# Performance work log

Hardware: AMD Instinct MI355X
Metric: run time of the kernel (lower is better)

## Reference

```python
import jax, jax.numpy as jnp
import numpy as np

FILTERS = 512
DQK = FILTERS // 8  # 64


def setup_inputs() -> dict:
    key = jax.random.key(0)
    ks = jax.random.split(key, 7)
    B, H, W, C = 32, 32, 32, FILTERS
    x = jax.random.normal(ks[0], (B, H, W, C), dtype=jnp.float32)
    # 1x1 convs == per-pixel dense layers: weight [Cin, Cout], bias [Cout]
    def glorot(k, cin, cout):
        lim = np.sqrt(6.0 / (cin + cout)).astype(np.float32)
        return jax.random.uniform(k, (cin, cout), jnp.float32, -lim, lim)
    return {
        "x": x,
        "wq": glorot(ks[1], C, DQK), "bq": jnp.zeros((DQK,), jnp.float32),
        "wk": glorot(ks[2], C, DQK), "bk": jnp.zeros((DQK,), jnp.float32),
        "wv": glorot(ks[3], C, C),   "bv": jnp.zeros((C,), jnp.float32),
    }


def reference(x, wq, bq, wk, bk, wv, bv):
    B, H, W, C = x.shape
    N = H * W
    xf = x.reshape(B, N, C)                       # flatten spatial -> tokens
    q = xf @ wq + bq                              # [B, N, C//8]
    k = xf @ wk + bk                              # [B, N, C//8]
    v = xf @ wv + bv                              # [B, N, C]
    scale = 1.0 / jnp.sqrt(jnp.float32(C // 8))
    scores = jnp.einsum('bnd,bmd->bnm', q, k) * scale  # [B, N, N]
    probs = jax.nn.softmax(scores, axis=-1)
    attended = jnp.einsum('bnm,bmc->bnc', probs, v)    # [B, N, C]
    return attended.reshape(B, H, W, C) + x
```

## Files before the change

### kernel.cpp

```cpp
#include <hip/hip_runtime.h>
#include <stdint.h>

#define B_ 32
#define N_ 1024
#define C_ 512
#define D_ 64

typedef __attribute__((ext_vector_type(8))) __bf16 bf8;
typedef __attribute__((ext_vector_type(4))) float f32x4;

typedef const __attribute__((address_space(1))) void* gp_t;
typedef __attribute__((address_space(3))) void* lp_t;

__device__ inline void g2l16(const void* g, void* l) {
    __builtin_amdgcn_global_load_lds((gp_t)g, (lp_t)l, 16, 0, 0);
}

__device__ inline float b2f(unsigned short u) {
    return __uint_as_float(((unsigned)u) << 16);
}
__device__ inline unsigned short f2b(float f) {
    unsigned u = __float_as_uint(f);
    u += 0x7FFF + ((u >> 16) & 1);
    return (unsigned short)(u >> 16);
}

#define MFMA16(a, b, c) __builtin_amdgcn_mfma_f32_16x16x32_bf16((a), (b), (c), 0, 0, 0)

__device__ __forceinline__ void ld_frags(const unsigned short* As, const unsigned short* Bs,
                                         int wm, int wn, int lane,
                                         bf8 (&a)[2][4], bf8 (&bb)[2][4]) {
    #pragma unroll
    for (int kq = 0; kq < 2; ++kq) {
        #pragma unroll
        for (int ti = 0; ti < 4; ++ti)
            a[kq][ti] = *(const bf8*)&As[((wm * 4 + ti) * 2 + kq) * 512 + lane * 8];
        #pragma unroll
        for (int tj = 0; tj < 4; ++tj)
            bb[kq][tj] = *(const bf8*)&Bs[((wn * 4 + tj) * 2 + kq) * 512 + lane * 8];
    }
}

__device__ __forceinline__ void do_mfma(const bf8 (&a)[2][4], const bf8 (&bb)[2][4],
                                        f32x4 (&acc)[4][4]) {
    #pragma unroll
    for (int kq = 0; kq < 2; ++kq)
        #pragma unroll
        for (int ti = 0; ti < 4; ++ti)
            #pragma unroll
            for (int tj = 0; tj < 4; ++tj)
                acc[ti][tj] = MFMA16(a[kq][ti], bb[kq][tj], acc[ti][tj]);
}

__global__ __launch_bounds__(256) void xcvt(const float* __restrict__ x,
                                            unsigned short* __restrict__ xb) {
    int i = blockIdx.x * 256 + threadIdx.x;
    float4 f = ((const float4*)x)[i];
    ushort4 o;
    o.x = f2b(f.x); o.y = f2b(f.y); o.z = f2b(f.z); o.w = f2b(f.w);
    ((ushort4*)xb)[i] = o;
}

__global__ __launch_bounds__(256) void wtrans_all(
    const float* __restrict__ wq, const float* __restrict__ wk,
    const float* __restrict__ wv, unsigned short* __restrict__ wt)
{
    int t = blockIdx.x * 256 + threadIdx.x;
    int co = t >> 9;
    int ci = t & 511;
    const float* src;
    int col, cout;
    if (co < 64)       { src = wq; col = co;       cout = 64;  }
    else if (co < 128) { src = wk; col = co - 64;  cout = 64;  }
    else               { src = wv; col = co - 128; cout = 512; }
    wt[t] = f2b(src[(size_t)ci * cout + col]);
}

__global__ __launch_bounds__(256) void qkv(
    const unsigned short* __restrict__ xb,
    const unsigned short* __restrict__ WT,
    const float* __restrict__ bq, const float* __restrict__ bk,
    const float* __restrict__ bv,
    unsigned short* __restrict__ q, unsigned short* __restrict__ k,
    unsigned short* __restrict__ vT)
{
    const int f_  = blockIdx.x;
    const int xcd = f_ & 7;
    const int s_  = f_ >> 3;
    const int rb  = xcd * 32 + s_ / 5;
    const int cb  = s_ % 5;

    const int tid = threadIdx.x;
    const int lane = tid & 63;
    const int wave = tid >> 6;
    const int wm = wave >> 1, wn = wave & 1;
    const int lr = lane & 15;
    const int lk = lane >> 4;

    __shared__ unsigned short SM[32768];
    unsigned short* TB = SM;

    const int row0 = rb * 128;
    const int col0 = cb * 128;

    f32x4 zero4 = {0.f, 0.f, 0.f, 0.f};
    f32x4 acc[4][4];
    #pragma unroll
    for (int i = 0; i < 4; ++i)
        #pragma unroll
        for (int j = 0; j < 4; ++j) acc[i][j] = zero4;

    auto stage = [&](int buf, int kk) {
        unsigned short* As = SM + buf * 8192;
        unsigned short* Bs = SM + 16384 + buf * 8192;
        #pragma unroll
        for (int i = 0; i < 4; ++i) {
            int f = wave * 4 + i;
            int t = f >> 1, kq = f & 1;
            g2l16(xb + (size_t)(row0 + t * 16 + lr) * C_ + kk + kq * 32 + lk * 8,
                  &As[f * 512]);
            g2l16(WT + (size_t)(col0 + t * 16 + lr) * C_ + kk + kq * 32 + lk * 8,
                  &Bs[f * 512]);
        }
    };

    stage(0, 0);
    stage(1, 64);
    int cur = 0;
    for (int t = 0; t < 6; ++t) {
        asm volatile("s_waitcnt vmcnt(8)" ::: "memory");
        __builtin_amdgcn_s_barrier();
        bf8 a[2][4], bb[2][4];
        ld_frags(SM + cur * 8192, SM + 16384 + cur * 8192, wm, wn, lane, a, bb);
        asm volatile("s_waitcnt lgkmcnt(0)" ::: "memory");
        __builtin_amdgcn_s_barrier();
        stage(cur, (t + 2) * 64);
        do_mfma(a, bb, acc);
        cur ^= 1;
    }
    {
        asm volatile("s_waitcnt vmcnt(8)" ::: "memory");
        __builtin_amdgcn_s_barrier();
        bf8 a[2][4], bb[2][4];
        ld_frags(SM + cur * 8192, SM + 16384 + cur * 8192, wm, wn, lane, a, bb);
        do_mfma(a, bb, acc);
        cur ^= 1;
    }
    {
        asm volatile("s_waitcnt vmcnt(0)" ::: "memory");
        __builtin_amdgcn_s_barrier();
        bf8 a[2][4], bb[2][4];
        ld_frags(SM + cur * 8192, SM + 16384 + cur * 8192, wm, wn, lane, a, bb);
        do_mfma(a, bb, acc);
    }

    if (cb == 0) {
        unsigned short* outp = (wn == 0) ? q : k;
        const float* bias = (wn == 0) ? bq : bk;
        #pragma unroll
        for (int ti = 0; ti < 4; ++ti)
            #pragma unroll
            for (int tj = 0; tj < 4; ++tj) {
                int col = tj * 16 + lr;
                float bi = bias[col];
                #pragma unroll
                for (int r = 0; r < 4; ++r) {
                    int row = row0 + wm * 64 + ti * 16 + lk * 4 + r;
                    outp[(size_t)row * D_ + col] = f2b(acc[ti][tj][r] + bi);
                }
            }
    } else {
        const int colv = (cb - 1) * 128;
        __syncthreads();
        #pragma unroll
        for (int ti = 0; ti < 4; ++ti)
            #pragma unroll
            for (int tj = 0; tj < 4; ++tj) {
                int c = wn * 64 + tj * 16 + lr;
                float bi = bv[colv + c];
                int tok = wm * 64 + ti * 16 + lk * 4;
                ushort4 o;
                o.x = f2b(acc[ti][tj][0] + bi);
                o.y = f2b(acc[ti][tj][1] + bi);
                o.z = f2b(acc[ti][tj][2] + bi);
                o.w = f2b(acc[ti][tj][3] + bi);
                *(ushort4*)&TB[c * 132 + tok] = o;
            }
        __syncthreads();
        const int b  = row0 >> 10;
        const int n0 = row0 & 1023;
        #pragma unroll
        for (int i = 0; i < 16; ++i) {
            int idx = tid + 256 * i;
            int c = idx >> 5, ch = idx & 31;
            ushort4 t4 = *(const ushort4*)&TB[c * 132 + ch * 4];
            *(ushort4*)&vT[((size_t)(b * C_ + colv + c)) * N_ + n0 + ch * 4] = t4;
        }
    }
}

#define SLD 1032
__global__ __launch_bounds__(256) void scores(
    const unsigned short* __restrict__ q,
    const unsigned short* __restrict__ k,
    unsigned short* __restrict__ P)
{
    const int f_  = blockIdx.x;
    const int xcd = f_ & 7;
    const int s_  = f_ >> 3;
    const int b   = xcd * 4 + (s_ >> 6);
    const int qt  = s_ & 63;

    const int tid = threadIdx.x, lane = tid & 63, wave = tid >> 6;
    const int lr = lane & 15, lk = lane >> 4;
    __shared__ unsigned short S[16 * SLD];

    const int n0 = qt * 16;
    const unsigned short* qrow = q + (size_t)(b * N_ + n0 + lr) * D_ + lk * 8;
    bf8 qa0 = *(const bf8*)(qrow);
    bf8 qa1 = *(const bf8*)(qrow + 32);

    const int m0w = wave * 256;
    #pragma unroll 4
    for (int mt = 0; mt < 16; ++mt) {
        int m = m0w + mt * 16;
        const unsigned short* krow = k + (size_t)(b * N_ + m + lr) * D_ + lk * 8;
        bf8 kb0 = *(const bf8*)(krow);
        bf8 kb1 = *(const bf8*)(krow + 32);
        f32x4 s = {0.f, 0.f, 0.f, 0.f};
        s = MFMA16(qa0, kb0, s);
        s = MFMA16(qa1, kb1, s);
        #pragma unroll
        for (int r = 0; r < 4; ++r)
            S[(lk * 4 + r) * SLD + m + lr] = f2b(s[r] * 0.125f);
    }
    __syncthreads();

    #pragma unroll
    for (int rr4 = 0; rr4 < 4; ++rr4) {
        int rr = wave * 4 + rr4;
        float vals[16];
        float mx = -1e30f;
        #pragma unroll
        for (int j = 0; j < 16; ++j) {
            vals[j] = b2f(S[rr * SLD + j * 64 + lane]);
            mx = fmaxf(mx, vals[j]);
        }
        #pragma unroll
        for (int off = 32; off; off >>= 1) mx = fmaxf(mx, __shfl_xor(mx, off));
        float sum = 0.f;
        #pragma unroll
        for (int j = 0; j < 16; ++j) { vals[j] = __expf(vals[j] - mx); sum += vals[j]; }
        #pragma unroll
        for (int off = 32; off; off >>= 1) sum += __shfl_xor(sum, off);
        float inv = 1.f / sum;
        unsigned short* pp = P + (size_t)(b * N_ + n0 + rr) * N_;
        #pragma unroll
        for (int j = 0; j < 16; ++j) pp[j * 64 + lane] = f2b(vals[j] * inv);
    }
}

__global__ __launch_bounds__(512, 2) void pv(
    const unsigned short* __restrict__ P,
    const unsigned short* __restrict__ vT,
    const float* __restrict__ x,
    float* __restrict__ out)
{
    const int f_   = blockIdx.x;
    const int xcd  = f_ & 7;
    const int s_   = f_ >> 3;
    const int b    = xcd * 4 + (s_ >> 3);
    const int w_   = s_ & 7;
    const int m0   = (w_ & 3) * 256;
    const int c0   = (w_ >> 2) * 256;

    const int tid = threadIdx.x, lane = tid & 63, wave = tid >> 6;
    const int wm = wave >> 2;
    const int wn = wave & 3;
    const int lr = lane & 15, lk = lane >> 4;

    __shared__ unsigned short SM[65536];

    f32x4 zero4 = {0.f, 0.f, 0.f, 0.f};
    f32x4 acc[8][4];
    #pragma unroll
    for (int i = 0; i < 8; ++i)
        #pragma unroll
        for (int j = 0; j < 4; ++j) acc[i][j] = zero4;

    const unsigned short* Pb = P  + (size_t)b * N_ * N_;
    const unsigned short* Vb = vT + (size_t)b * C_ * N_;

    auto stage = [&](int t32) {
        unsigned short* As = SM + (t32 & 3) * 16384;
        unsigned short* Bs = As + 8192;
        const int kk = t32 * 32;
        #pragma unroll
        for (int i = 0; i < 2; ++i) {
            int f = wave * 2 + i;
            g2l16(Pb + (size_t)(m0 + f * 16 + lr) * N_ + kk + lk * 8, &As[f * 512]);
            g2l16(Vb + (size_t)(c0 + f * 16 + lr) * N_ + kk + lk * 8, &Bs[f * 512]);
        }
    };

    auto compute = [&](int t32) {
        const unsigned short* As = SM + (t32 & 3) * 16384;
        const unsigned short* Bs = As + 8192;
        bf8 a[8], bb[4];
        #pragma unroll
        for (int ti = 0; ti < 8; ++ti)
            a[ti] = *(const bf8*)&As[(wm * 8 + ti) * 512 + lane * 8];
        #pragma unroll
        for (int tj = 0; tj < 4; ++tj)
            bb[tj] = *(const bf8*)&Bs[(wn * 4 + tj) * 512 + lane * 8];
        asm volatile("s_waitcnt lgkmcnt(0)" ::: "memory");
        __builtin_amdgcn_sched_barrier(0);
        __builtin_amdgcn_s_setprio(1);
        #pragma unroll
        for (int ti = 0; ti < 8; ++ti)
            #pragma unroll
            for (int tj = 0; tj < 4; ++tj)
                acc[ti][tj] = MFMA16(a[ti], bb[tj], acc[ti][tj]);
        __builtin_amdgcn_s_setprio(0);
    };

    stage(0); stage(1); stage(2);
    for (int t = 0; t < 29; ++t) {
        asm volatile("s_waitcnt vmcnt(8)" ::: "memory");
        __builtin_amdgcn_s_barrier();
        stage(t + 3);
        compute(t);
    }
    {
        asm volatile("s_waitcnt vmcnt(8)" ::: "memory");
        __builtin_amdgcn_s_barrier();
        compute(29);
    }
    {
        asm volatile("s_waitcnt vmcnt(4)" ::: "memory");
        __builtin_amdgcn_s_barrier();
        compute(30);
    }
    {
        asm volatile("s_waitcnt vmcnt(0)" ::: "memory");
        __builtin_amdgcn_s_barrier();
        compute(31);
    }

    #pragma unroll
    for (int ti = 0; ti < 8; ++ti)
        #pragma unroll
        for (int tj = 0; tj < 4; ++tj) {
            int col = c0 + wn * 64 + tj * 16 + lr;
            #pragma unroll
            for (int r = 0; r < 4; ++r) {
                int row = m0 + wm * 128 + ti * 16 + lk * 4 + r;
                size_t idx = (size_t)(b * N_ + row) * C_ + col;
                out[idx] = acc[ti][tj][r] + x[idx];
            }
        }
}

extern "C" void kernel_launch(void* const* d_in, const int* in_sizes, int n_in,
                              void* d_out, int out_size, void* d_ws, size_t ws_size,
                              hipStream_t stream) {
    (void)in_sizes; (void)n_in; (void)out_size; (void)ws_size;
    const float* xf = (const float*)d_in[0];
    const float* wq = (const float*)d_in[1];
    const float* bq = (const float*)d_in[2];
    const float* wk = (const float*)d_in[3];
    const float* bk = (const float*)d_in[4];
    const float* wv = (const float*)d_in[5];
    const float* bv = (const float*)d_in[6];
    float* out = (float*)d_out;

    char* ws = (char*)d_ws;
    unsigned short* qb  = (unsigned short*)(ws);
    unsigned short* kb  = (unsigned short*)(ws + 4194304);
    unsigned short* vTb = (unsigned short*)(ws + 8388608);
    unsigned short* WT  = (unsigned short*)(ws + 41943040);
    unsigned short* xb  = (unsigned short*)(ws + 42598400);
    unsigned short* Pb  = (unsigned short*)(ws + 41943040);

    xcvt<<<16384, 256, 0, stream>>>(xf, xb);
    wtrans_all<<<1280, 256, 0, stream>>>(wq, wk, wv, WT);
    qkv<<<1280, 256, 0, stream>>>(xb, WT, bq, bk, bv, qb, kb, vTb);
    scores<<<2048, 256, 0, stream>>>(qb, kb, Pb);
    pv<<<256, 512, 0, stream>>>(Pb, vTb, xf, out);
}
```

Measured before the change: 265.3 us.

## Shrink PV tiles to 256x128 with triple buffering and fuse prep kernels

The PV kernel now computes 256x128 output tiles instead of 256x256 and launches twice as many blocks. Each wave holds half as many accumulators, and the LDS ring drops from four stages to three, so launch bounds can ask for four blocks per CU. The goal is more occupancy and better latency hiding, at the cost of reloading each P tile twice. Separately, the x-conversion and weight-transpose kernels are merged into one launch to save a kernel launch.

Result: no change. 265.6 us (+0.1%).

```diff
diff --git a/kernel.cpp b/kernel.cpp
--- a/kernel.cpp
+++ b/kernel.cpp
@@ -52,28 +52,29 @@
                 acc[ti][tj] = MFMA16(a[kq][ti], bb[kq][tj], acc[ti][tj]);
 }
 
-__global__ __launch_bounds__(256) void xcvt(const float* __restrict__ x,
-                                            unsigned short* __restrict__ xb) {
-    int i = blockIdx.x * 256 + threadIdx.x;
-    float4 f = ((const float4*)x)[i];
-    ushort4 o;
-    o.x = f2b(f.x); o.y = f2b(f.y); o.z = f2b(f.z); o.w = f2b(f.w);
-    ((ushort4*)xb)[i] = o;
-}
-
-__global__ __launch_bounds__(256) void wtrans_all(
+__global__ __launch_bounds__(256) void prep(
+    const float* __restrict__ x, unsigned short* __restrict__ xb,
     const float* __restrict__ wq, const float* __restrict__ wk,
     const float* __restrict__ wv, unsigned short* __restrict__ wt)
 {
-    int t = blockIdx.x * 256 + threadIdx.x;
-    int co = t >> 9;
-    int ci = t & 511;
-    const float* src;
-    int col, cout;
-    if (co < 64)       { src = wq; col = co;       cout = 64;  }
-    else if (co < 128) { src = wk; col = co - 64;  cout = 64;  }
-    else               { src = wv; col = co - 128; cout = 512; }
-    wt[t] = f2b(src[(size_t)ci * cout + col]);
+    int bid = blockIdx.x;
+    if (bid < 16384) {
+        int i = bid * 256 + threadIdx.x;
+        float4 f = ((const float4*)x)[i];
+        ushort4 o;
+        o.x = f2b(f.x); o.y = f2b(f.y); o.z = f2b(f.z); o.w = f2b(f.w);
+        ((ushort4*)xb)[i] = o;
+    } else {
+        int t = (bid - 16384) * 256 + threadIdx.x;
+        int co = t >> 9;
+        int ci = t & 511;
+        const float* src;
+        int col, cout;
+        if (co < 64)       { src = wq; col = co;       cout = 64;  }
+        else if (co < 128) { src = wk; col = co - 64;  cout = 64;  }
+        else               { src = wv; col = co - 128; cout = 512; }
+        wt[t] = f2b(src[(size_t)ci * cout + col]);
+    }
 }
 
 __global__ __launch_bounds__(256) void qkv(
@@ -260,7 +261,7 @@
     }
 }
 
-__global__ __launch_bounds__(512, 2) void pv(
+__global__ __launch_bounds__(512, 4) void pv(
     const unsigned short* __restrict__ P,
     const unsigned short* __restrict__ vT,
     const float* __restrict__ x,
@@ -269,92 +270,97 @@
     const int f_   = blockIdx.x;
     const int xcd  = f_ & 7;
     const int s_   = f_ >> 3;
-    const int b    = xcd * 4 + (s_ >> 3);
-    const int w_   = s_ & 7;
+    const int b    = xcd * 4 + (s_ >> 4);
+    const int w_   = s_ & 15;
     const int m0   = (w_ & 3) * 256;
-    const int c0   = (w_ >> 2) * 256;
+    const int c0   = (w_ >> 2) * 128;
 
     const int tid = threadIdx.x, lane = tid & 63, wave = tid >> 6;
-    const int wm = wave >> 2;
-    const int wn = wave & 3;
+    const int wm = wave >> 1;
+    const int wn = wave & 1;
     const int lr = lane & 15, lk = lane >> 4;
 
-    __shared__ unsigned short SM[65536];
+    __shared__ unsigned short SM[36864];
 
     f32x4 zero4 = {0.f, 0.f, 0.f, 0.f};
-    f32x4 acc[8][4];
-    #pragma unroll
-    for (int i = 0; i < 8; ++i)
+    f32x4 acc[4][4];
+    #pragma unroll
+    for (int i = 0; i < 4; ++i)
         #pragma unroll
         for (int j = 0; j < 4; ++j) acc[i][j] = zero4;
 
     const unsigned short* Pb = P  + (size_t)b * N_ * N_;
     const unsigned short* Vb = vT + (size_t)b * C_ * N_;
 
-    auto stage = [&](int t32) {
-        unsigned short* As = SM + (t32 & 3) * 16384;
-        unsigned short* Bs = As + 8192;
+    auto stage = [&](int t32, int buf) {
+        unsigned short* Ab = SM + buf * 12288;
+        unsigned short* Bb = Ab + 8192;
         const int kk = t32 * 32;
         #pragma unroll
-        for (int i = 0; i < 2; ++i) {
-            int f = wave * 2 + i;
-            g2l16(Pb + (size_t)(m0 + f * 16 + lr) * N_ + kk + lk * 8, &As[f * 512]);
-            g2l16(Vb + (size_t)(c0 + f * 16 + lr) * N_ + kk + lk * 8, &Bs[f * 512]);
+        for (int i = 0; i < 3; ++i) {
+            int f = wave * 3 + i;
+            if (f < 16) {
+                g2l16(Pb + (size_t)(m0 + f * 16 + lr) * N_ + kk + lk * 8,
+                      &Ab[f * 512]);
+            } else {
+                int g = f - 16;
+                g2l16(Vb + (size_t)(c0 + g * 16 + lr) * N_ + kk + lk * 8,
+                      &Bb[g * 512]);
+            }
         }
     };
 
-    auto compute = [&](int t32) {
-        const unsigned short* As = SM + (t32 & 3) * 16384;
-        const unsigned short* Bs = As + 8192;
-        bf8 a[8], bb[4];
-        #pragma unroll
-        for (int ti = 0; ti < 8; ++ti)
-            a[ti] = *(const bf8*)&As[(wm * 8 + ti) * 512 + lane * 8];
+    auto compute = [&](int buf) {
+        const unsigned short* Ab = SM + buf * 12288;
+        const unsigned short* Bb = Ab + 8192;
+        bf8 a[4], bb[4];
+        #pragma unroll
+        for (int ti = 0; ti < 4; ++ti)
+            a[ti] = *(const bf8*)&Ab[(wm * 4 + ti) * 512 + lane * 8];
         #pragma unroll
         for (int tj = 0; tj < 4; ++tj)
-            bb[tj] = *(const bf8*)&Bs[(wn * 4 + tj) * 512 + lane * 8];
+            bb[tj] = *(const bf8*)&Bb[(wn * 4 + tj) * 512 + lane * 8];
         asm volatile("s_waitcnt lgkmcnt(0)" ::: "memory");
         __builtin_amdgcn_sched_barrier(0);
         __builtin_amdgcn_s_setprio(1);
         #pragma unroll
-        for (int ti = 0; ti < 8; ++ti)
+        for (int ti = 0; ti < 4; ++ti)
             #pragma unroll
             for (int tj = 0; tj < 4; ++tj)
                 acc[ti][tj] = MFMA16(a[ti], bb[tj], acc[ti][tj]);
         __builtin_amdgcn_s_setprio(0);
     };
 
-    stage(0); stage(1); stage(2);
-    for (int t = 0; t < 29; ++t) {
-        asm volatile("s_waitcnt vmcnt(8)" ::: "memory");
-        __builtin_amdgcn_s_barrier();
-        stage(t + 3);
-        compute(t);
+    stage(0, 0); stage(1, 1);
+    int bufc = 0;
+    for (int t = 0; t < 30; ++t) {
+        asm volatile("s_waitcnt vmcnt(3)" ::: "memory");
+        __builtin_amdgcn_s_barrier();
+        int bufs = bufc + 2; if (bufs >= 3) bufs -= 3;
+        stage(t + 2, bufs);
+        compute(bufc);
+        bufc = bufc + 1; if (bufc >= 3) bufc -= 3;
     }
     {
-        asm volatile("s_waitcnt vmcnt(8)" ::: "memory");
-        __builtin_amdgcn_s_barrier();
-        compute(29);
-    }
-    {
-        asm volatile("s_waitcnt vmcnt(4)" ::: "memory");
-        __builtin_amdgcn_s_barrier();
-        compute(30);
+        asm volatile("s_waitcnt vmcnt(3)" ::: "memory");
+        __builtin_amdgcn_s_barrier();
+        compute(bufc);
+        bufc = bufc + 1; if (bufc >= 3) bufc -= 3;
     }
     {
         asm volatile("s_waitcnt vmcnt(0)" ::: "memory");
         __builtin_amdgcn_s_barrier();
-        compute(31);
-    }
-
-    #pragma unroll
-    for (int ti = 0; ti < 8; ++ti)
+        compute(bufc);
+    }
+
+    #pragma unroll
+    for (int ti = 0; ti < 4; ++ti)
         #pragma unroll
         for (int tj = 0; tj < 4; ++tj) {
             int col = c0 + wn * 64 + tj * 16 + lr;
             #pragma unroll
             for (int r = 0; r < 4; ++r) {
-                int row = m0 + wm * 128 + ti * 16 + lk * 4 + r;
+                int row = m0 + wm * 64 + ti * 16 + lk * 4 + r;
                 size_t idx = (size_t)(b * N_ + row) * C_ + col;
                 out[idx] = acc[ti][tj][r] + x[idx];
             }
@@ -382,9 +388,8 @@
     unsigned short* xb  = (unsigned short*)(ws + 42598400);
     unsigned short* Pb  = (unsigned short*)(ws + 41943040);
 
-    xcvt<<<16384, 256, 0, stream>>>(xf, xb);
-    wtrans_all<<<1280, 256, 0, stream>>>(wq, wk, wv, WT);
+    prep<<<17664, 256, 0, stream>>>(xf, xb, wq, wk, wv, WT);
     qkv<<<1280, 256, 0, stream>>>(xb, WT, bq, bk, bv, qb, kb, vTb);
     scores<<<2048, 256, 0, stream>>>(qb, kb, Pb);
-    pv<<<256, 512, 0, stream>>>(Pb, vTb, xf, out);
-}
+    pv<<<512, 512, 0, stream>>>(Pb, vTb, xf, out);
+}
```
